# Kernel optimization log

Measured on AMD Instinct MI355X. Metric: run time of the kernel, lower is better.

## Reference

```python
import jax, jax.numpy as jnp
import numpy as np

N_EMBD = 1024
NUM_HEADS = 16
HEAD_DIM = N_EMBD // NUM_HEADS
B, N = 4, 1024
EPS = 1e-5


def _ln(x, w, b):
    mu = jnp.mean(x, axis=-1, keepdims=True)
    var = jnp.var(x, axis=-1, keepdims=True)
    return (x - mu) * jax.lax.rsqrt(var + EPS) * w + b


def setup_inputs() -> dict:
    key = jax.random.key(0)
    ks = jax.random.split(key, 12)
    s = 0.02
    d, dff = N_EMBD, 4 * N_EMBD
    return {
        "x": jax.random.normal(ks[0], (B, N, d), dtype=jnp.float32),
        "ln1_w": jnp.ones((d,), jnp.float32),
        "ln1_b": jnp.zeros((d,), jnp.float32),
        "Wq": jax.random.normal(ks[1], (d, d), jnp.float32) * s,
        "bq": jnp.zeros((d,), jnp.float32),
        "Wk": jax.random.normal(ks[2], (d, d), jnp.float32) * s,
        "bk": jnp.zeros((d,), jnp.float32),
        "Wv": jax.random.normal(ks[3], (d, d), jnp.float32) * s,
        "bv": jnp.zeros((d,), jnp.float32),
        "Wo": jax.random.normal(ks[4], (d, d), jnp.float32) * s,
        "bo": jnp.zeros((d,), jnp.float32),
        "ln2_w": jnp.ones((d,), jnp.float32),
        "ln2_b": jnp.zeros((d,), jnp.float32),
        "Wfc": jax.random.normal(ks[5], (d, dff), jnp.float32) * s,
        "bfc": jnp.zeros((dff,), jnp.float32),
        "Wproj": jax.random.normal(ks[6], (dff, d), jnp.float32) * s,
        "bproj": jnp.zeros((d,), jnp.float32),
    }


def reference(x, ln1_w, ln1_b, Wq, bq, Wk, bk, Wv, bv, Wo, bo,
              ln2_w, ln2_b, Wfc, bfc, Wproj, bproj):
    # --- attention sublayer ---
    h = _ln(x, ln1_w, ln1_b)  # [B,N,D]
    q = (h @ Wq + bq).reshape(B, N, NUM_HEADS, HEAD_DIM).transpose(0, 2, 1, 3)
    k = (h @ Wk + bk).reshape(B, N, NUM_HEADS, HEAD_DIM).transpose(0, 2, 1, 3)
    v = (h @ Wv + bv).reshape(B, N, NUM_HEADS, HEAD_DIM).transpose(0, 2, 1, 3)
    scale = 1.0 / np.sqrt(HEAD_DIM).astype(np.float32)
    attn = jax.nn.softmax(jnp.einsum("bhqd,bhkd->bhqk", q, k) * scale, axis=-1)
    o = jnp.einsum("bhqk,bhkd->bhqd", attn, v)  # [B,H,N,Dh]
    o = o.transpose(0, 2, 1, 3).reshape(B, N, N_EMBD)
    x = x + (o @ Wo + bo)
    # --- MLP sublayer (exact GELU, matching torch nn.GELU default) ---
    h2 = _ln(x, ln2_w, ln2_b)
    h2 = jax.nn.gelu(h2 @ Wfc + bfc, approximate=False)
    x = x + (h2 @ Wproj + bproj)
    return x
```

## Files before the change

kernel.cpp:

```cpp
#include <hip/hip_runtime.h>
#include <hip/hip_bf16.h>

typedef unsigned short u16;
typedef u16 u16x8 __attribute__((ext_vector_type(8)));
typedef u16 u16x4 __attribute__((ext_vector_type(4)));
typedef __bf16 bf16x8 __attribute__((ext_vector_type(8)));
typedef float f32x4 __attribute__((ext_vector_type(4)));

__device__ __forceinline__ u16 f2bf(float f) {
  union { __hip_bfloat16 h; u16 u; } cv;
  cv.h = __float2bfloat16(f);
  return cv.u;
}

__device__ __forceinline__ void glds16(const void* g, void* l) {
  __builtin_amdgcn_global_load_lds(
      (const __attribute__((address_space(1))) unsigned int*)g,
      (__attribute__((address_space(3))) unsigned int*)l, 16, 0, 0);
}

__global__ __launch_bounds__(256) void transpose_bf16(const float* __restrict__ W,
                                                      u16* __restrict__ Wt,
                                                      int K, int N) {
  __shared__ float tile[32][33];
  int tx = threadIdx.x, ty = threadIdx.y;
  int n0 = blockIdx.x * 32, k0 = blockIdx.y * 32;
#pragma unroll
  for (int j = 0; j < 4; ++j)
    tile[ty + j * 8][tx] = W[(size_t)(k0 + ty + j * 8) * N + n0 + tx];
  __syncthreads();
#pragma unroll
  for (int j = 0; j < 4; ++j)
    Wt[(size_t)(n0 + ty + j * 8) * K + k0 + tx] = f2bf(tile[tx][ty + j * 8]);
}

__global__ __launch_bounds__(256) void ln_kernel(const float* __restrict__ x,
                                                 const float* __restrict__ w,
                                                 const float* __restrict__ b,
                                                 u16* __restrict__ out) {
  int row = blockIdx.x, t = threadIdx.x;
  const float* xr = x + (size_t)row * 1024;
  float4 v = *reinterpret_cast<const float4*>(xr + t * 4);
  float s = v.x + v.y + v.z + v.w;
  float s2 = v.x * v.x + v.y * v.y + v.z * v.z + v.w * v.w;
#pragma unroll
  for (int m = 1; m < 64; m <<= 1) {
    s += __shfl_xor(s, m, 64);
    s2 += __shfl_xor(s2, m, 64);
  }
  __shared__ float red[8];
  if ((t & 63) == 0) { red[t >> 6] = s; red[(t >> 6) + 4] = s2; }
  __syncthreads();
  s = red[0] + red[1] + red[2] + red[3];
  s2 = red[4] + red[5] + red[6] + red[7];
  float mu = s * (1.f / 1024.f);
  float var = s2 * (1.f / 1024.f) - mu * mu;
  float rs = rsqrtf(var + 1e-5f);
  float4 wv = *reinterpret_cast<const float4*>(w + t * 4);
  float4 bv = *reinterpret_cast<const float4*>(b + t * 4);
  u16x4 o;
  o.x = f2bf((v.x - mu) * rs * wv.x + bv.x);
  o.y = f2bf((v.y - mu) * rs * wv.y + bv.y);
  o.z = f2bf((v.z - mu) * rs * wv.z + bv.z);
  o.w = f2bf((v.w - mu) * rs * wv.w + bv.w);
  *reinterpret_cast<u16x4*>(out + (size_t)row * 1024 + t * 4) = o;
}

template <int MODE, int TN>
__global__ __launch_bounds__(256) void gemm_k(
    const u16* __restrict__ A, const u16* __restrict__ Bt,
    const float* __restrict__ b0, const float* __restrict__ b1,
    const float* __restrict__ b2, const float* __restrict__ res,
    u16* __restrict__ o0, u16* __restrict__ o1, u16* __restrict__ vt,
    float* __restrict__ of, int M, int N, int K, float qscale) {
  constexpr int WHALF = TN / 2;
  constexpr int NF = TN / 32;
  __shared__ u16 As[2][128 * 32];
  __shared__ u16 Bs[2][TN * 32];
  const int tid = threadIdx.x;
  const int lane = tid & 63, w = tid >> 6;
  const int wr = w >> 1, wc = w & 1;
  const int l15 = lane & 15, l4 = lane >> 4;
  const int row0 = blockIdx.x * 128, col0 = blockIdx.y * TN;
  f32x4 acc[4][NF];
#pragma unroll
  for (int m = 0; m < 4; ++m)
#pragma unroll
    for (int n = 0; n < NF; ++n) acc[m][n] = (f32x4){0.f, 0.f, 0.f, 0.f};

  auto stage = [&](int buf, int k0) {
#pragma unroll
    for (int i = 0; i < 2; ++i) {
      int c = i * 256 + tid;
      glds16(A + (size_t)(row0 + (c >> 2)) * K + k0 + (c & 3) * 8, &As[buf][c * 8]);
    }
    if constexpr (TN == 128) {
#pragma unroll
      for (int i = 0; i < 2; ++i) {
        int c = i * 256 + tid;
        glds16(Bt + (size_t)(col0 + (c >> 2)) * K + k0 + (c & 3) * 8, &Bs[buf][c * 8]);
      }
    } else {
      int c = tid;
      glds16(Bt + (size_t)(col0 + (c >> 2)) * K + k0 + (c & 3) * 8, &Bs[buf][c * 8]);
    }
  };

  stage(0, 0);
  __syncthreads();
  const int nk = K >> 5;
  for (int t = 0; t < nk; ++t) {
    int cur = t & 1;
    if (t + 1 < nk) stage(cur ^ 1, (t + 1) << 5);
    bf16x8 af[4], bfr[NF];
#pragma unroll
    for (int m = 0; m < 4; ++m)
      af[m] = *reinterpret_cast<const bf16x8*>(&As[cur][(wr * 64 + m * 16 + l15) * 32 + l4 * 8]);
#pragma unroll
    for (int n = 0; n < NF; ++n)
      bfr[n] = *reinterpret_cast<const bf16x8*>(&Bs[cur][(wc * WHALF + n * 16 + l15) * 32 + l4 * 8]);
#pragma unroll
    for (int m = 0; m < 4; ++m)
#pragma unroll
      for (int n = 0; n < NF; ++n)
        acc[m][n] = __builtin_amdgcn_mfma_f32_16x16x32_bf16(af[m], bfr[n], acc[m][n], 0, 0, 0);
    __syncthreads();
  }

  if constexpr (MODE == 0) {
    const int which = (int)(blockIdx.y >> 3);
    const int bidx = (int)(blockIdx.x >> 3);
#pragma unroll
    for (int m = 0; m < 4; ++m)
#pragma unroll
      for (int n = 0; n < NF; ++n) {
        int colc = (col0 & 1023) + wc * WHALF + n * 16 + l15;
        int hh = colc >> 6, d = colc & 63;
        int nb = (row0 & 1023) + wr * 64 + m * 16 + l4 * 4;
        if (which == 2) {
          u16x4 pk;
#pragma unroll
          for (int r = 0; r < 4; ++r) pk[r] = f2bf(acc[m][n][r] + b2[colc]);
          *reinterpret_cast<u16x4*>(
              vt + (((size_t)(bidx * 16 + hh) * 64 + d) * 1024 + nb)) = pk;
        } else {
          const float* bb = (which == 0) ? b0 : b1;
          u16* dst = (which == 0) ? o0 : o1;
          float sc = (which == 0) ? qscale : 1.0f;
#pragma unroll
          for (int r = 0; r < 4; ++r)
            dst[((size_t)(bidx * 16 + hh) * 1024 + nb + r) * 64 + d] =
                f2bf((acc[m][n][r] + bb[colc]) * sc);
        }
      }
  } else {
#pragma unroll
    for (int m = 0; m < 4; ++m)
#pragma unroll
      for (int n = 0; n < NF; ++n)
#pragma unroll
        for (int r = 0; r < 4; ++r) {
          int row = row0 + wr * 64 + m * 16 + l4 * 4 + r;
          int col = col0 + wc * WHALF + n * 16 + l15;
          float val = acc[m][n][r];
          if constexpr (MODE == 1) {
            of[(size_t)row * N + col] = val + b0[col] + res[(size_t)row * N + col];
          } else {
            val += b0[col];
            float g = 0.5f * val * (1.0f + erff(val * 0.70710678118f));
            o0[(size_t)row * N + col] = f2bf(g);
          }
        }
  }
}

__global__ __launch_bounds__(256) void attn_kernel(const u16* __restrict__ q,
                                                   const u16* __restrict__ k,
                                                   const u16* __restrict__ vt,
                                                   u16* __restrict__ o) {
  const int bh = blockIdx.x, qb = blockIdx.y;
  const int b = bh >> 4, h = bh & 15;
  __shared__ u16 Ks[2][4096];
  __shared__ u16 Vt[2][4096];
  __shared__ u16 Ps[4][1024];
  const int tid = threadIdx.x, lane = tid & 63, w = tid >> 6;
  const int l15 = lane & 15, l4 = lane >> 4;
  const int sw = l15 & 7;
  const u16* kbase = k + (size_t)bh * 65536;
  const u16* vtbase = vt + (size_t)bh * 65536;

  const u16* qrow = q + ((size_t)bh * 1024 + qb * 64 + w * 16 + l15) * 64;
  bf16x8 qf0 = *reinterpret_cast<const bf16x8*>(qrow + l4 * 8);
  bf16x8 qf1 = *reinterpret_cast<const bf16x8*>(qrow + 32 + l4 * 8);

  auto stageKV = [&](int buf, int kv0) {
#pragma unroll
    for (int i = 0; i < 2; ++i) {
      int c = i * 256 + tid, r = c >> 3, sl = (c & 7) ^ (r & 7);
      glds16(kbase + (size_t)(kv0 + r) * 64 + sl * 8, &Ks[buf][c * 8]);
    }
#pragma unroll
    for (int i = 0; i < 2; ++i) {
      int c = i * 256 + tid, r = c >> 3, sl = (c & 7) ^ (r & 7);
      glds16(vtbase + (size_t)r * 1024 + kv0 + sl * 8, &Vt[buf][c * 8]);
    }
  };

  f32x4 oacc[4];
#pragma unroll
  for (int n = 0; n < 4; ++n) oacc[n] = (f32x4){0.f, 0.f, 0.f, 0.f};
  float mrow[4], lrow[4];
#pragma unroll
  for (int r = 0; r < 4; ++r) { mrow[r] = -3.0e38f; lrow[r] = 0.f; }

  stageKV(0, 0);
  __syncthreads();

  for (int kv0 = 0; kv0 < 1024; kv0 += 64) {
    int cur = (kv0 >> 6) & 1;
    if (kv0 + 64 < 1024) stageKV(cur ^ 1, kv0 + 64);

    f32x4 st[4];
#pragma unroll
    for (int t = 0; t < 4; ++t) {
      int row = t * 16 + l15;
      f32x4 s = (f32x4){0.f, 0.f, 0.f, 0.f};
      bf16x8 kf0 = *reinterpret_cast<const bf16x8*>(&Ks[cur][row * 64 + ((l4 ^ sw) << 3)]);
      s = __builtin_amdgcn_mfma_f32_16x16x32_bf16(qf0, kf0, s, 0, 0, 0);
      bf16x8 kf1 = *reinterpret_cast<const bf16x8*>(&Ks[cur][row * 64 + (((4 + l4) ^ sw) << 3)]);
      s = __builtin_amdgcn_mfma_f32_16x16x32_bf16(qf1, kf1, s, 0, 0, 0);
      st[t] = s;
    }

    float tmax[4];
#pragma unroll
    for (int r = 0; r < 4; ++r)
      tmax[r] = fmaxf(fmaxf(st[0][r], st[1][r]), fmaxf(st[2][r], st[3][r]));
#pragma unroll
    for (int md = 1; md < 16; md <<= 1)
#pragma unroll
      for (int r = 0; r < 4; ++r) tmax[r] = fmaxf(tmax[r], __shfl_xor(tmax[r], md, 64));
    float pr[4][4], alpha[4], rsum[4];
#pragma unroll
    for (int r = 0; r < 4; ++r) {
      float mnew = fmaxf(mrow[r], tmax[r]);
      alpha[r] = exp2f(mrow[r] - mnew);
      mrow[r] = mnew;
#pragma unroll
      for (int t = 0; t < 4; ++t) pr[t][r] = exp2f(st[t][r] - mnew);
      rsum[r] = (pr[0][r] + pr[1][r]) + (pr[2][r] + pr[3][r]);
    }
#pragma unroll
    for (int md = 1; md < 16; md <<= 1)
#pragma unroll
      for (int r = 0; r < 4; ++r) rsum[r] += __shfl_xor(rsum[r], md, 64);
#pragma unroll
    for (int r = 0; r < 4; ++r) lrow[r] = lrow[r] * alpha[r] + rsum[r];
#pragma unroll
    for (int n = 0; n < 4; ++n)
#pragma unroll
      for (int r = 0; r < 4; ++r) oacc[n][r] *= alpha[r];

#pragma unroll
    for (int t = 0; t < 4; ++t)
#pragma unroll
      for (int r = 0; r < 4; ++r) {
        int qq = l4 * 4 + r, kv = t * 16 + l15;
        Ps[w][qq * 64 + ((((kv >> 3) ^ (qq & 7)) << 3) | (kv & 7))] = f2bf(pr[t][r]);
      }

#pragma unroll
    for (int c2 = 0; c2 < 2; ++c2) {
      bf16x8 pf = *reinterpret_cast<const bf16x8*>(
          &Ps[w][l15 * 64 + ((((c2 << 2) + l4) ^ sw) << 3)]);
#pragma unroll
      for (int n = 0; n < 4; ++n) {
        bf16x8 vf = *reinterpret_cast<const bf16x8*>(
            &Vt[cur][(n * 16 + l15) * 64 + ((((c2 << 2) + l4) ^ sw) << 3)]);
        oacc[n] = __builtin_amdgcn_mfma_f32_16x16x32_bf16(pf, vf, oacc[n], 0, 0, 0);
      }
    }
    __syncthreads();
  }

  float invl[4];
#pragma unroll
  for (int r = 0; r < 4; ++r) invl[r] = 1.0f / lrow[r];
#pragma unroll
  for (int n = 0; n < 4; ++n)
#pragma unroll
    for (int r = 0; r < 4; ++r) {
      int nr = qb * 64 + w * 16 + l4 * 4 + r;
      int dc = n * 16 + l15;
      o[((size_t)(b * 1024 + nr)) * 1024 + h * 64 + dc] = f2bf(oacc[n][r] * invl[r]);
    }
}

extern "C" void kernel_launch(void* const* d_in, const int* in_sizes, int n_in,
                              void* d_out, int out_size, void* d_ws, size_t ws_size,
                              hipStream_t stream) {
  (void)in_sizes; (void)n_in; (void)out_size; (void)ws_size;
  const float* x     = (const float*)d_in[0];
  const float* ln1w  = (const float*)d_in[1];
  const float* ln1b  = (const float*)d_in[2];
  const float* Wq    = (const float*)d_in[3];
  const float* bq    = (const float*)d_in[4];
  const float* Wk    = (const float*)d_in[5];
  const float* bk    = (const float*)d_in[6];
  const float* Wv    = (const float*)d_in[7];
  const float* bv    = (const float*)d_in[8];
  const float* Wo    = (const float*)d_in[9];
  const float* bo    = (const float*)d_in[10];
  const float* ln2w  = (const float*)d_in[11];
  const float* ln2b  = (const float*)d_in[12];
  const float* Wfc   = (const float*)d_in[13];
  const float* bfc   = (const float*)d_in[14];
  const float* Wproj = (const float*)d_in[15];
  const float* bproj = (const float*)d_in[16];
  float* out = (float*)d_out;

  char* p = (char*)d_ws;
  u16* hb     = (u16*)p; p += (size_t)4096 * 1024 * 2;
  u16* WqkvT  = (u16*)p; p += (size_t)3072 * 1024 * 2;
  u16* WoT    = (u16*)p; p += (size_t)1024 * 1024 * 2;
  u16* WfcT   = (u16*)p; p += (size_t)4096 * 1024 * 2;
  u16* WprojT = (u16*)p; p += (size_t)1024 * 4096 * 2;
  u16* qb_    = (u16*)p; p += (size_t)4096 * 1024 * 2;
  u16* kb_    = (u16*)p; p += (size_t)4096 * 1024 * 2;
  u16* vt_    = (u16*)p; p += (size_t)4096 * 1024 * 2;
  u16* ob_    = (u16*)p; p += (size_t)4096 * 1024 * 2;
  float* x1   = (float*)p; p += (size_t)4096 * 1024 * 4;
  u16* h2     = (u16*)p; p += (size_t)4096 * 1024 * 2;
  u16* ffnb   = (u16*)p; p += (size_t)4096 * 4096 * 2;

  const float qscale = 0.125f * 1.44269504089f;

  dim3 tb(32, 8);
  transpose_bf16<<<dim3(32, 32), tb, 0, stream>>>(Wq, WqkvT, 1024, 1024);
  transpose_bf16<<<dim3(32, 32), tb, 0, stream>>>(Wk, WqkvT + (size_t)1024 * 1024, 1024, 1024);
  transpose_bf16<<<dim3(32, 32), tb, 0, stream>>>(Wv, WqkvT + (size_t)2048 * 1024, 1024, 1024);
  transpose_bf16<<<dim3(32, 32), tb, 0, stream>>>(Wo, WoT, 1024, 1024);
  transpose_bf16<<<dim3(128, 32), tb, 0, stream>>>(Wfc, WfcT, 1024, 4096);
  transpose_bf16<<<dim3(32, 128), tb, 0, stream>>>(Wproj, WprojT, 4096, 1024);

  ln_kernel<<<4096, 256, 0, stream>>>(x, ln1w, ln1b, hb);

  gemm_k<0, 128><<<dim3(32, 24), 256, 0, stream>>>(hb, WqkvT, bq, bk, bv, nullptr,
                                                   qb_, kb_, vt_, nullptr,
                                                   4096, 3072, 1024, qscale);

  attn_kernel<<<dim3(64, 16), 256, 0, stream>>>(qb_, kb_, vt_, ob_);

  gemm_k<1, 64><<<dim3(32, 16), 256, 0, stream>>>(ob_, WoT, bo, nullptr, nullptr, x,
                                                  nullptr, nullptr, nullptr, x1,
                                                  4096, 1024, 1024, 1.f);

  ln_kernel<<<4096, 256, 0, stream>>>(x1, ln2w, ln2b, h2);

  gemm_k<2, 128><<<dim3(32, 32), 256, 0, stream>>>(h2, WfcT, bfc, nullptr, nullptr, nullptr,
                                                   ffnb, nullptr, nullptr, nullptr,
                                                   4096, 4096, 1024, 1.f);

  gemm_k<1, 64><<<dim3(32, 16), 256, 0, stream>>>(ffnb, WprojT, bproj, nullptr, nullptr, x1,
                                                  nullptr, nullptr, nullptr, out,
                                                  4096, 1024, 4096, 1.f);
}
```

Before: 391.5 us.

## Use 256x256-tile 8-wave GEMM with split-K for projection and reduce kernel

Adds a 512-thread GEMM kernel with 256x256 output tiles, a swizzled LDS layout, direct global-to-LDS loads, split-phase double buffering with explicit waitcnt and barriers, and MFMA priority raising. It replaces the QKV, FC+GELU and down-projection GEMMs. The down projection is split-K into four bf16 partials, which a new reduce kernel sums together with the bias and residual. The goal is more reuse per tile and enough workgroups for the narrow projection GEMM. In exchange it adds extra partial-buffer traffic and rounds each partial sum to bf16.

```diff
diff --git a/kernel.cpp b/kernel.cpp
--- a/kernel.cpp
+++ b/kernel.cpp
@@ -11,6 +11,11 @@
   union { __hip_bfloat16 h; u16 u; } cv;
   cv.h = __float2bfloat16(f);
   return cv.u;
+}
+__device__ __forceinline__ float bf2f(u16 u) {
+  union { unsigned u; float f; } c;
+  c.u = ((unsigned)u) << 16;
+  return c.f;
 }
 
 __device__ __forceinline__ void glds16(const void* g, void* l) {
@@ -66,13 +71,220 @@
   *reinterpret_cast<u16x4*>(out + (size_t)row * 1024 + t * 4) = o;
 }
 
+template <int MODE>
+__global__ __launch_bounds__(512, 2) void gemm256(
+    const u16* __restrict__ A, const u16* __restrict__ Bt,
+    const float* __restrict__ b0, const float* __restrict__ b1,
+    const float* __restrict__ b2,
+    u16* __restrict__ o0, u16* __restrict__ o1, u16* __restrict__ o2,
+    int Kfull, int KL, int MT, int NT, float qscale) {
+  __shared__ u16 lds[2][2][2][256 * 32];
+  const int tid = threadIdx.x;
+  const int lane = tid & 63, w = tid >> 6;
+  const int wm = w >> 2, wn = w & 3;
+  const int l15 = lane & 15, l4 = lane >> 4;
+  const int skey = (l15 >> 1) & 3;
+
+  const int nwg = gridDim.x;
+  int wg = (int)blockIdx.x;
+  wg = (wg & 7) * (nwg >> 3) + (wg >> 3);
+  const int mt = wg % MT;
+  int rest = wg / MT;
+  const int nt = rest % NT;
+  const int zt = rest / NT;
+
+  const int row0 = mt * 256, col0 = nt * 256;
+  const int kbase = zt * KL;
+  const int nkt = KL >> 6;
+
+  auto stage = [&](int buf, int op, int ks, int kt) {
+    const u16* src = op ? Bt : A;
+    const int base = op ? col0 : row0;
+    const int kb = kbase + (kt << 6) + (ks << 5);
+    u16* dst = &lds[buf][op][ks][0];
+#pragma unroll
+    for (int i = 0; i < 2; ++i) {
+      int c = i * 512 + tid;
+      int r = c >> 2, ch = c & 3;
+      int sch = ch ^ ((r >> 1) & 3);
+      glds16(src + (size_t)(base + r) * Kfull + kb + sch * 8, dst + c * 8);
+    }
+  };
+  auto rdA = [&](int buf, int ks, int m) -> bf16x8 {
+    int row = wm * 128 + m * 16 + l15;
+    return *reinterpret_cast<const bf16x8*>(&lds[buf][0][ks][row * 32 + ((l4 ^ skey) << 3)]);
+  };
+  auto rdB = [&](int buf, int ks, int n) -> bf16x8 {
+    int row = wn * 64 + n * 16 + l15;
+    return *reinterpret_cast<const bf16x8*>(&lds[buf][1][ks][row * 32 + ((l4 ^ skey) << 3)]);
+  };
+
+  f32x4 acc[8][4];
+#pragma unroll
+  for (int m = 0; m < 8; ++m)
+#pragma unroll
+    for (int n = 0; n < 4; ++n) acc[m][n] = (f32x4){0.f, 0.f, 0.f, 0.f};
+
+  stage(0, 0, 0, 0);
+  stage(0, 0, 1, 0);
+  stage(0, 1, 0, 0);
+  stage(0, 1, 1, 0);
+  asm volatile("s_waitcnt vmcnt(2)" ::: "memory");
+  __builtin_amdgcn_s_barrier();
+
+  bf16x8 af[8];
+  for (int t = 0; t < nkt; ++t) {
+    const int cur = t & 1, nxt = cur ^ 1;
+    const bool pf = (t + 1 < nkt);
+    {
+#pragma unroll
+      for (int m = 0; m < 8; ++m) af[m] = rdA(cur, 0, m);
+      bf16x8 bq0 = rdB(cur, 0, 0), bq1 = rdB(cur, 0, 1);
+      if (pf) stage(nxt, 0, 0, t + 1);
+      __builtin_amdgcn_s_barrier();
+      __builtin_amdgcn_s_setprio(1);
+#pragma unroll
+      for (int m = 0; m < 8; ++m) {
+        acc[m][0] = __builtin_amdgcn_mfma_f32_16x16x32_bf16(af[m], bq0, acc[m][0], 0, 0, 0);
+        acc[m][1] = __builtin_amdgcn_mfma_f32_16x16x32_bf16(af[m], bq1, acc[m][1], 0, 0, 0);
+      }
+      __builtin_amdgcn_s_setprio(0);
+      __builtin_amdgcn_s_barrier();
+    }
+    {
+      bf16x8 bq2 = rdB(cur, 0, 2), bq3 = rdB(cur, 0, 3);
+      if (pf) {
+        stage(nxt, 0, 1, t + 1);
+        asm volatile("s_waitcnt vmcnt(4)" ::: "memory");
+      } else {
+        asm volatile("s_waitcnt vmcnt(0)" ::: "memory");
+      }
+      __builtin_amdgcn_s_barrier();
+      __builtin_amdgcn_s_setprio(1);
+#pragma unroll
+      for (int m = 0; m < 8; ++m) {
+        acc[m][2] = __builtin_amdgcn_mfma_f32_16x16x32_bf16(af[m], bq2, acc[m][2], 0, 0, 0);
+        acc[m][3] = __builtin_amdgcn_mfma_f32_16x16x32_bf16(af[m], bq3, acc[m][3], 0, 0, 0);
+      }
+      __builtin_amdgcn_s_setprio(0);
+      __builtin_amdgcn_s_barrier();
+    }
+    {
+#pragma unroll
+      for (int m = 0; m < 8; ++m) af[m] = rdA(cur, 1, m);
+      bf16x8 bq0 = rdB(cur, 1, 0), bq1 = rdB(cur, 1, 1);
+      if (pf) stage(nxt, 1, 0, t + 1);
+      __builtin_amdgcn_s_barrier();
+      __builtin_amdgcn_s_setprio(1);
+#pragma unroll
+      for (int m = 0; m < 8; ++m) {
+        acc[m][0] = __builtin_amdgcn_mfma_f32_16x16x32_bf16(af[m], bq0, acc[m][0], 0, 0, 0);
+        acc[m][1] = __builtin_amdgcn_mfma_f32_16x16x32_bf16(af[m], bq1, acc[m][1], 0, 0, 0);
+      }
+      __builtin_amdgcn_s_setprio(0);
+      __builtin_amdgcn_s_barrier();
+    }
+    {
+      bf16x8 bq2 = rdB(cur, 1, 2), bq3 = rdB(cur, 1, 3);
+      if (pf) stage(nxt, 1, 1, t + 1);
+      asm volatile("s_waitcnt vmcnt(2)" ::: "memory");
+      __builtin_amdgcn_s_barrier();
+      __builtin_amdgcn_s_setprio(1);
+#pragma unroll
+      for (int m = 0; m < 8; ++m) {
+        acc[m][2] = __builtin_amdgcn_mfma_f32_16x16x32_bf16(af[m], bq2, acc[m][2], 0, 0, 0);
+        acc[m][3] = __builtin_amdgcn_mfma_f32_16x16x32_bf16(af[m], bq3, acc[m][3], 0, 0, 0);
+      }
+      __builtin_amdgcn_s_setprio(0);
+      __builtin_amdgcn_s_barrier();
+    }
+  }
+
+  if constexpr (MODE == 0) {
+    const int which = nt >> 2;
+    const int bidx = mt >> 2;
+#pragma unroll
+    for (int m = 0; m < 8; ++m)
+#pragma unroll
+      for (int n = 0; n < 4; ++n) {
+        int colc = (col0 & 1023) + wn * 64 + n * 16 + l15;
+        int hh = colc >> 6, d = colc & 63;
+        int nb = (row0 & 1023) + wm * 128 + m * 16 + l4 * 4;
+        if (which == 2) {
+          u16x4 pk;
+#pragma unroll
+          for (int r = 0; r < 4; ++r) pk[r] = f2bf(acc[m][n][r] + b2[colc]);
+          *reinterpret_cast<u16x4*>(o2 + (((size_t)(bidx * 16 + hh) * 64 + d) * 1024 + nb)) = pk;
+        } else {
+          const float* bb = (which == 0) ? b0 : b1;
+          u16* dst = (which == 0) ? o0 : o1;
+          float sc = (which == 0) ? qscale : 1.0f;
+#pragma unroll
+          for (int r = 0; r < 4; ++r)
+            dst[((size_t)(bidx * 16 + hh) * 1024 + nb + r) * 64 + d] =
+                f2bf((acc[m][n][r] + bb[colc]) * sc);
+        }
+      }
+  } else if constexpr (MODE == 2) {
+    const int N = NT * 256;
+#pragma unroll
+    for (int m = 0; m < 8; ++m)
+#pragma unroll
+      for (int n = 0; n < 4; ++n)
+#pragma unroll
+        for (int r = 0; r < 4; ++r) {
+          int row = row0 + wm * 128 + m * 16 + l4 * 4 + r;
+          int col = col0 + wn * 64 + n * 16 + l15;
+          float val = acc[m][n][r] + b0[col];
+          float g = 0.5f * val * (1.0f + erff(val * 0.70710678118f));
+          o0[(size_t)row * N + col] = f2bf(g);
+        }
+  } else {
+    const int M = MT * 256, N = NT * 256;
+    u16* base = o0 + (size_t)zt * M * N;
+#pragma unroll
+    for (int m = 0; m < 8; ++m)
+#pragma unroll
+      for (int n = 0; n < 4; ++n)
+#pragma unroll
+        for (int r = 0; r < 4; ++r) {
+          int row = row0 + wm * 128 + m * 16 + l4 * 4 + r;
+          int col = col0 + wn * 64 + n * 16 + l15;
+          base[(size_t)row * N + col] = f2bf(acc[m][n][r]);
+        }
+  }
+}
+
+__global__ __launch_bounds__(256) void proj_reduce(const u16* __restrict__ parts,
+                                                   const float* __restrict__ bias,
+                                                   const float* __restrict__ res,
+                                                   float* __restrict__ out) {
+  size_t i = ((size_t)blockIdx.x * 256 + threadIdx.x) * 8;
+  int col = (int)(i & 1023);
+  float s[8];
+  float4 r0 = *reinterpret_cast<const float4*>(res + i);
+  float4 r1 = *reinterpret_cast<const float4*>(res + i + 4);
+  s[0] = r0.x; s[1] = r0.y; s[2] = r0.z; s[3] = r0.w;
+  s[4] = r1.x; s[5] = r1.y; s[6] = r1.z; s[7] = r1.w;
+#pragma unroll
+  for (int j = 0; j < 8; ++j) s[j] += bias[col + j];
+#pragma unroll
+  for (int sp = 0; sp < 4; ++sp) {
+    u16x8 pv = *reinterpret_cast<const u16x8*>(parts + (size_t)sp * 4096 * 1024 + i);
+#pragma unroll
+    for (int j = 0; j < 8; ++j) s[j] += bf2f(pv[j]);
+  }
+  float4 o0 = {s[0], s[1], s[2], s[3]};
+  float4 o1 = {s[4], s[5], s[6], s[7]};
+  *reinterpret_cast<float4*>(out + i) = o0;
+  *reinterpret_cast<float4*>(out + i + 4) = o1;
+}
+
 template <int MODE, int TN>
 __global__ __launch_bounds__(256) void gemm_k(
     const u16* __restrict__ A, const u16* __restrict__ Bt,
-    const float* __restrict__ b0, const float* __restrict__ b1,
-    const float* __restrict__ b2, const float* __restrict__ res,
-    u16* __restrict__ o0, u16* __restrict__ o1, u16* __restrict__ vt,
-    float* __restrict__ of, int M, int N, int K, float qscale) {
+    const float* __restrict__ b0, const float* __restrict__ res,
+    float* __restrict__ of, int M, int N, int K) {
   constexpr int WHALF = TN / 2;
   constexpr int NF = TN / 32;
   __shared__ u16 As[2][128 * 32];
@@ -127,51 +339,16 @@
     __syncthreads();
   }
 
-  if constexpr (MODE == 0) {
-    const int which = (int)(blockIdx.y >> 3);
-    const int bidx = (int)(blockIdx.x >> 3);
-#pragma unroll
-    for (int m = 0; m < 4; ++m)
-#pragma unroll
-      for (int n = 0; n < NF; ++n) {
-        int colc = (col0 & 1023) + wc * WHALF + n * 16 + l15;
-        int hh = colc >> 6, d = colc & 63;
-        int nb = (row0 & 1023) + wr * 64 + m * 16 + l4 * 4;
-        if (which == 2) {
-          u16x4 pk;
-#pragma unroll
-          for (int r = 0; r < 4; ++r) pk[r] = f2bf(acc[m][n][r] + b2[colc]);
-          *reinterpret_cast<u16x4*>(
-              vt + (((size_t)(bidx * 16 + hh) * 64 + d) * 1024 + nb)) = pk;
-        } else {
-          const float* bb = (which == 0) ? b0 : b1;
-          u16* dst = (which == 0) ? o0 : o1;
-          float sc = (which == 0) ? qscale : 1.0f;
-#pragma unroll
-          for (int r = 0; r < 4; ++r)
-            dst[((size_t)(bidx * 16 + hh) * 1024 + nb + r) * 64 + d] =
-                f2bf((acc[m][n][r] + bb[colc]) * sc);
-        }
-      }
-  } else {
-#pragma unroll
-    for (int m = 0; m < 4; ++m)
-#pragma unroll
-      for (int n = 0; n < NF; ++n)
-#pragma unroll
-        for (int r = 0; r < 4; ++r) {
-          int row = row0 + wr * 64 + m * 16 + l4 * 4 + r;
-          int col = col0 + wc * WHALF + n * 16 + l15;
-          float val = acc[m][n][r];
-          if constexpr (MODE == 1) {
-            of[(size_t)row * N + col] = val + b0[col] + res[(size_t)row * N + col];
-          } else {
-            val += b0[col];
-            float g = 0.5f * val * (1.0f + erff(val * 0.70710678118f));
-            o0[(size_t)row * N + col] = f2bf(g);
-          }
-        }
-  }
+#pragma unroll
+  for (int m = 0; m < 4; ++m)
+#pragma unroll
+    for (int n = 0; n < NF; ++n)
+#pragma unroll
+      for (int r = 0; r < 4; ++r) {
+        int row = row0 + wr * 64 + m * 16 + l4 * 4 + r;
+        int col = col0 + wc * WHALF + n * 16 + l15;
+        of[(size_t)row * N + col] = acc[m][n][r] + b0[col] + res[(size_t)row * N + col];
+      }
 }
 
 __global__ __launch_bounds__(256) void attn_kernel(const u16* __restrict__ q,
@@ -345,23 +522,19 @@
 
   ln_kernel<<<4096, 256, 0, stream>>>(x, ln1w, ln1b, hb);
 
-  gemm_k<0, 128><<<dim3(32, 24), 256, 0, stream>>>(hb, WqkvT, bq, bk, bv, nullptr,
-                                                   qb_, kb_, vt_, nullptr,
-                                                   4096, 3072, 1024, qscale);
+  gemm256<0><<<192, 512, 0, stream>>>(hb, WqkvT, bq, bk, bv,
+                                      qb_, kb_, vt_, 1024, 1024, 16, 12, qscale);
 
   attn_kernel<<<dim3(64, 16), 256, 0, stream>>>(qb_, kb_, vt_, ob_);
 
-  gemm_k<1, 64><<<dim3(32, 16), 256, 0, stream>>>(ob_, WoT, bo, nullptr, nullptr, x,
-                                                  nullptr, nullptr, nullptr, x1,
-                                                  4096, 1024, 1024, 1.f);
+  gemm_k<1, 64><<<dim3(32, 16), 256, 0, stream>>>(ob_, WoT, bo, x, x1, 4096, 1024, 1024);
 
   ln_kernel<<<4096, 256, 0, stream>>>(x1, ln2w, ln2b, h2);
 
-  gemm_k<2, 128><<<dim3(32, 32), 256, 0, stream>>>(h2, WfcT, bfc, nullptr, nullptr, nullptr,
-                                                   ffnb, nullptr, nullptr, nullptr,
-                                                   4096, 4096, 1024, 1.f);
-
-  gemm_k<1, 64><<<dim3(32, 16), 256, 0, stream>>>(ffnb, WprojT, bproj, nullptr, nullptr, x1,
-                                                  nullptr, nullptr, nullptr, out,
-                                                  4096, 1024, 4096, 1.f);
-}
+  gemm256<2><<<256, 512, 0, stream>>>(h2, WfcT, bfc, nullptr, nullptr,
+                                      ffnb, nullptr, nullptr, 1024, 1024, 16, 16, 1.f);
+
+  gemm256<3><<<256, 512, 0, stream>>>(ffnb, WprojT, nullptr, nullptr, nullptr,
+                                      qb_, nullptr, nullptr, 4096, 1024, 16, 4, 1.f);
+  proj_reduce<<<2048, 256, 0, stream>>>(qb_, bproj, x1, out);
+}
```

After: 376.2 us. 3.9% less time.
